# Kernel optimization log

Hardware: AMD Instinct MI355X
Metric: run time of the kernel (lower is better)

## Reference

```python
import jax, jax.numpy as jnp
import numpy as np

DIM = 1024
HEADS = 16
HEAD_DIM = DIM // HEADS
BLOCK = 32
FEAT = 128
EPS = 1e-8


def setup_inputs() -> dict:
    key = jax.random.key(0)
    ks = jax.random.split(key, 5)
    b, n = 4, 4096
    x = jax.random.normal(ks[0], (b, n, DIM), dtype=jnp.float32)
    Wqkv = jax.random.normal(ks[1], (DIM, 3 * DIM), dtype=jnp.float32) / np.sqrt(DIM)
    proj = jax.random.normal(ks[2], (HEADS, HEAD_DIM, FEAT), dtype=jnp.float32) / np.sqrt(HEAD_DIM)
    Wout = jax.random.normal(ks[3], (DIM, DIM), dtype=jnp.float32) / np.sqrt(DIM)
    bout = jnp.zeros((DIM,), dtype=jnp.float32)
    return {"x": x, "Wqkv": Wqkv, "proj": proj, "Wout": Wout, "bout": bout}


def reference(x, Wqkv, proj, Wout, bout):
    b, n, d = x.shape
    h, dh = HEADS, HEAD_DIM
    nb = n // BLOCK
    qkv = x @ Wqkv                                    # [b, n, 3d]
    q, k, v = jnp.split(qkv, 3, axis=-1)
    # [b, h, nb, bs, dh]
    def to_blocks(t):
        return t.reshape(b, nb, BLOCK, h, dh).transpose(0, 3, 1, 2, 4)
    q, k, v = to_blocks(q), to_blocks(k), to_blocks(v)
    # per-head feature projection + elu feature map
    qf = jax.nn.elu(jnp.einsum('bhmsd,hdf->bhmsf', q, proj)) + 1.0
    kf = jax.nn.elu(jnp.einsum('bhmsd,hdf->bhmsf', k, proj)) + 1.0
    kv = jnp.einsum('bhmsf,bhmsd->bhmfd', kf, v)      # per-block kv state
    out = jnp.einsum('bhmsf,bhmfd->bhmsd', qf, kv)
    z = 1.0 / (jnp.einsum('bhmsf,bhmf->bhms', qf, kf.sum(axis=3)) + EPS)
    out = out * z[..., None]
    out = out.transpose(0, 2, 3, 1, 4).reshape(b, n, d)  # [b, n, d]
    return out @ Wout + bout
```

## Files before the change

### kernel.cpp

```cpp
#include <hip/hip_runtime.h>
#include <stdint.h>


typedef unsigned short u16;
typedef __attribute__((ext_vector_type(4))) float f32x4;
typedef __attribute__((ext_vector_type(8))) __bf16 bf16x8;
typedef __attribute__((ext_vector_type(8))) u16 us8;
typedef __attribute__((ext_vector_type(4))) u16 us4;

#define GLOAD_LDS16(g, l)                                                      \
  __builtin_amdgcn_global_load_lds(                                            \
      (const __attribute__((address_space(1))) void*)(g),                      \
      (__attribute__((address_space(3))) void*)(l), 16, 0, 0)

__device__ __forceinline__ u16 f2bf(float f) {
  union { float f; unsigned u; } x; x.f = f;
  return (u16)((x.u + 0x7fffu + ((x.u >> 16) & 1u)) >> 16);
}

__device__ __forceinline__ bf16x8 ld8(const void* p) {
  return __builtin_bit_cast(bf16x8, *(const us8*)p);
}

__device__ __forceinline__ f32x4 mfma16(bf16x8 a, bf16x8 b, f32x4 c) {
  return __builtin_amdgcn_mfma_f32_16x16x32_bf16(a, b, c, 0, 0, 0);
}

__global__ void cast_bf16_k(const float* __restrict__ in, u16* __restrict__ out,
                            int n4) {
  int stride = gridDim.x * blockDim.x;
  for (int i = blockIdx.x * blockDim.x + threadIdx.x; i < n4; i += stride) {
    f32x4 v = ((const f32x4*)in)[i];
    us4 o;
    o[0] = f2bf(v[0]); o[1] = f2bf(v[1]); o[2] = f2bf(v[2]); o[3] = f2bf(v[3]);
    ((us4*)out)[i] = o;
  }
}

__global__ __launch_bounds__(256)
void tcast_k(const float* __restrict__ in, u16* __restrict__ out, int R, int C) {
  __shared__ float tile[32][33];
  int tx = threadIdx.x & 31, ty = threadIdx.x >> 5;
  int r0 = blockIdx.y * 32, c0 = blockIdx.x * 32;
#pragma unroll
  for (int i = 0; i < 32; i += 8)
    tile[ty + i][tx] = in[(size_t)(r0 + ty + i) * C + c0 + tx];
  __syncthreads();
#pragma unroll
  for (int i = 0; i < 32; i += 8)
    out[(size_t)(c0 + ty + i) * R + r0 + tx] = f2bf(tile[tx][ty + i]);
}

__global__ __launch_bounds__(256)
void tcastv_k(const float* __restrict__ Wqkv, u16* __restrict__ dst) {
  __shared__ float tile[32][33];
  int tx = threadIdx.x & 31, ty = threadIdx.x >> 5;
  int e0 = blockIdx.y * 32, j0 = blockIdx.x * 32;
#pragma unroll
  for (int i = 0; i < 32; i += 8)
    tile[ty + i][tx] = Wqkv[(size_t)(e0 + ty + i) * 3072 + 2048 + j0 + tx];
  __syncthreads();
#pragma unroll
  for (int i = 0; i < 32; i += 8)
    dst[(size_t)(j0 + ty + i) * 1024 + e0 + tx] = f2bf(tile[tx][ty + i]);
}

__global__ __launch_bounds__(256)
void wqpb_k(const float* __restrict__ Wqkv, const float* __restrict__ proj,
            u16* __restrict__ BtAll) {
  __shared__ float pl[64][128];
  const int ec = blockIdx.x, h = blockIdx.y, qk = blockIdx.z;
  const float* ph = proj + (size_t)h * 8192;
  for (int i = threadIdx.x; i < 2048; i += 256)
    ((f32x4*)&pl[0][0])[i] = ((const f32x4*)ph)[i];
  __syncthreads();
  const int e = ec * 128 + (threadIdx.x >> 1);
  const int f0 = (threadIdx.x & 1) * 64;
  float wrow[64];
  const float* src = Wqkv + (size_t)e * 3072 + qk * 1024 + h * 64;
#pragma unroll
  for (int i = 0; i < 16; ++i)
    *(f32x4*)&wrow[i * 4] = *(const f32x4*)&src[i * 4];
  u16* dst = BtAll + (size_t)(qk * 2048 + h * 128) * 1024 + e;
  for (int fg = 0; fg < 16; ++fg) {
    f32x4 acc = (f32x4){0.f, 0.f, 0.f, 0.f};
    const int f = f0 + fg * 4;
#pragma unroll
    for (int d = 0; d < 64; ++d) {
      f32x4 p = *(f32x4*)&pl[d][f];
      acc += wrow[d] * p;
    }
#pragma unroll
    for (int u = 0; u < 4; ++u) dst[(size_t)(f + u) * 1024] = f2bf(acc[u]);
  }
}

template <int EPI>
__global__ __launch_bounds__(512, 1)
void gemm8p_k(const u16* __restrict__ A, int lda,
              const u16* __restrict__ Bt, int ldb,
              const float* __restrict__ bias,
              u16* __restrict__ o_qkf, u16* __restrict__ o_v,
              float* __restrict__ o_f32, int K, int ntx) {
  __shared__ __align__(16) char lds[131072];
  const int tid = threadIdx.x, lane = tid & 63, w = tid >> 6;
  const int wm = w >> 2, wn = w & 3;
  const int lr = lane & 15, lg = lane >> 4;
  const int cpx = (int)gridDim.x >> 3;
  const int bid = blockIdx.x;
  const int s = (bid & 7) * cpx + (bid >> 3);
  const int bxN = (s % ntx) * 256;
  const int byM = (s / ntx) * 256;
  const int nt = K >> 6;

  const int srow = w * 8 + (lane >> 3);
  const int scol = ((lane & 7) ^ ((lane >> 3) & 7)) * 8;

  auto stg = [&](const u16* src, int ld, int row0, int kt, int dstoff) {
#pragma unroll
    for (int j = 0; j < 2; ++j)
      GLOAD_LDS16(src + (size_t)(row0 + j * 64 + srow) * ld + kt + scol,
                  lds + dstoff + j * 8192 + w * 1024);
  };
  auto stgA0 = [&](int t) { stg(A, lda, byM, t * 64, (t & 1) * 65536); };
  auto stgA1 = [&](int t) { stg(A, lda, byM + 128, t * 64, (t & 1) * 65536 + 16384); };
  auto stgB0 = [&](int t) { stg(Bt, ldb, bxN, t * 64, (t & 1) * 65536 + 32768); };
  auto stgB1 = [&](int t) { stg(Bt, ldb, bxN + 128, t * 64, (t & 1) * 65536 + 49152); };

  f32x4 acc[8][4];
#pragma unroll
  for (int i = 0; i < 8; ++i)
#pragma unroll
    for (int j = 0; j < 4; ++j) acc[i][j] = (f32x4){0.f, 0.f, 0.f, 0.f};

  stgA0(0); stgA1(0); stgB0(0); stgB1(0);
  if (nt > 1) {
    stgB0(1); stgB1(1);
    asm volatile("s_waitcnt vmcnt(4)" ::: "memory");
  } else {
    asm volatile("s_waitcnt vmcnt(0)" ::: "memory");
  }
  __builtin_amdgcn_s_barrier();

  for (int t = 0; t < nt; ++t) {
    const char* Ab = lds + (t & 1) * 65536 + wm * 16384;
    const char* Bb = lds + (t & 1) * 65536 + 32768 + (wn >> 1) * 16384;
    const int brow = (wn & 1) * 64;
    bf16x8 a2[4][2], b2[4][2];

#pragma unroll
    for (int i = 0; i < 4; ++i)
#pragma unroll
      for (int ks = 0; ks < 2; ++ks) {
        int row = i * 16 + lr;
        a2[i][ks] = ld8(Ab + row * 128 + ((ks * 64 + lg * 16) ^ ((row & 7) << 4)));
      }
#pragma unroll
    for (int j = 0; j < 2; ++j)
#pragma unroll
      for (int ks = 0; ks < 2; ++ks) {
        int row = brow + j * 16 + lr;
        b2[j][ks] = ld8(Bb + row * 128 + ((ks * 64 + lg * 16) ^ ((row & 7) << 4)));
      }
    if (t + 1 < nt) stgA0(t + 1);
    __builtin_amdgcn_s_barrier();
    asm volatile("s_waitcnt lgkmcnt(0)" ::: "memory");
    __builtin_amdgcn_sched_barrier(0);
    __builtin_amdgcn_s_setprio(1);
#pragma unroll
    for (int i = 0; i < 4; ++i)
#pragma unroll
      for (int j = 0; j < 2; ++j)
#pragma unroll
        for (int ks = 0; ks < 2; ++ks)
          acc[i][j] = mfma16(a2[i][ks], b2[j][ks], acc[i][j]);
    __builtin_amdgcn_s_setprio(0);
    __builtin_amdgcn_s_barrier();

#pragma unroll
    for (int j = 2; j < 4; ++j)
#pragma unroll
      for (int ks = 0; ks < 2; ++ks) {
        int row = brow + j * 16 + lr;
        b2[j][ks] = ld8(Bb + row * 128 + ((ks * 64 + lg * 16) ^ ((row & 7) << 4)));
      }
    if (t + 1 < nt) stgA1(t + 1);
    __builtin_amdgcn_s_barrier();
    asm volatile("s_waitcnt lgkmcnt(0)" ::: "memory");
    __builtin_amdgcn_sched_barrier(0);
    __builtin_amdgcn_s_setprio(1);
#pragma unroll
    for (int i = 0; i < 4; ++i)
#pragma unroll
      for (int j = 2; j < 4; ++j)
#pragma unroll
        for (int ks = 0; ks < 2; ++ks)
          acc[i][j] = mfma16(a2[i][ks], b2[j][ks], acc[i][j]);
    __builtin_amdgcn_s_setprio(0);
    __builtin_amdgcn_s_barrier();

#pragma unroll
    for (int i = 0; i < 4; ++i)
#pragma unroll
      for (int ks = 0; ks < 2; ++ks) {
        int row = (4 + i) * 16 + lr;
        a2[i][ks] = ld8(Ab + row * 128 + ((ks * 64 + lg * 16) ^ ((row & 7) << 4)));
      }
    if (t + 2 < nt) stgB0(t + 2);
    __builtin_amdgcn_s_barrier();
    asm volatile("s_waitcnt lgkmcnt(0)" ::: "memory");
    __builtin_amdgcn_sched_barrier(0);
    __builtin_amdgcn_s_setprio(1);
#pragma unroll
    for (int i = 0; i < 4; ++i)
#pragma unroll
      for (int j = 0; j < 2; ++j)
#pragma unroll
        for (int ks = 0; ks < 2; ++ks)
          acc[4 + i][j] = mfma16(a2[i][ks], b2[j][ks], acc[4 + i][j]);
    __builtin_amdgcn_s_setprio(0);
    __builtin_amdgcn_s_barrier();

    if (t + 2 < nt) stgB1(t + 2);
    if (t < nt - 2)
      asm volatile("s_waitcnt vmcnt(4)" ::: "memory");
    else
      asm volatile("s_waitcnt vmcnt(0)" ::: "memory");
    __builtin_amdgcn_s_barrier();
    __builtin_amdgcn_s_setprio(1);
#pragma unroll
    for (int i = 0; i < 4; ++i)
#pragma unroll
      for (int j = 2; j < 4; ++j)
#pragma unroll
        for (int ks = 0; ks < 2; ++ks)
          acc[4 + i][j] = mfma16(a2[i][ks], b2[j][ks], acc[4 + i][j]);
    __builtin_amdgcn_s_setprio(0);
    __builtin_amdgcn_s_barrier();
  }

  const bool doelu = (EPI == 0) && (bxN < 4096);
#pragma unroll
  for (int mi = 0; mi < 8; ++mi)
#pragma unroll
    for (int nj = 0; nj < 4; ++nj) {
      const int col = bxN + wn * 64 + nj * 16 + lr;
#pragma unroll
      for (int rr = 0; rr < 4; ++rr) {
        const int row = byM + wm * 128 + mi * 16 + lg * 4 + rr;
        float x = acc[mi][nj][rr];
        if (EPI == 0) {
          if (doelu) {
            float v = x > 0.f ? x + 1.f : __expf(x);
            o_qkf[(size_t)row * 4096 + col] = f2bf(v);
          } else {
            o_v[(size_t)row * 1024 + (col - 4096)] = f2bf(x);
          }
        } else {
          o_f32[(size_t)row * 1024 + col] = x + bias[col];
        }
      }
    }
}

__global__ __launch_bounds__(64)
void attn_lite_k(const u16* __restrict__ qkf, u16* __restrict__ vbuf) {
  __shared__ __align__(16) u16 V_l[32 * 72];
  __shared__ __align__(16) u16 S_l[32 * 32];
  const int lane = threadIdx.x;
  const int bid = blockIdx.x;
  const int m = bid & 127, h = (bid >> 7) & 15, b = bid >> 11;
  const size_t t0 = (size_t)b * 4096 + (size_t)m * 32;
  const u16* qf = qkf + t0 * 4096 + h * 128;
  const u16* kf = qf + 2048;
  u16* vv = vbuf + t0 * 1024 + h * 64;
  const int lr = lane & 15, lg = lane >> 4;

#pragma unroll
  for (int it = 0; it < 4; ++it) {
    int s2 = it * 8 + (lane >> 3);
    int d0 = (lane & 7) * 8;
    *(us8*)&V_l[s2 * 72 + d0] = *(const us8*)&vv[(size_t)s2 * 1024 + d0];
  }

  f32x4 sacc[2][2];
#pragma unroll
  for (int mm = 0; mm < 2; ++mm)
#pragma unroll
    for (int nn = 0; nn < 2; ++nn) sacc[mm][nn] = (f32x4){0.f, 0.f, 0.f, 0.f};
#pragma unroll
  for (int ks = 0; ks < 4; ++ks) {
    bf16x8 aq[2], bk[2];
#pragma unroll
    for (int mm = 0; mm < 2; ++mm) {
      aq[mm] = ld8(&qf[(size_t)(mm * 16 + lr) * 4096 + ks * 32 + lg * 8]);
      bk[mm] = ld8(&kf[(size_t)(mm * 16 + lr) * 4096 + ks * 32 + lg * 8]);
    }
#pragma unroll
    for (int mm = 0; mm < 2; ++mm)
#pragma unroll
      for (int nn = 0; nn < 2; ++nn)
        sacc[mm][nn] = mfma16(aq[mm], bk[nn], sacc[mm][nn]);
  }

  float rs[2][4];
#pragma unroll
  for (int mm = 0; mm < 2; ++mm)
#pragma unroll
    for (int r = 0; r < 4; ++r) {
      float t = sacc[mm][0][r] + sacc[mm][1][r];
      t += __shfl_xor(t, 1);
      t += __shfl_xor(t, 2);
      t += __shfl_xor(t, 4);
      t += __shfl_xor(t, 8);
      rs[mm][r] = t;
    }

#pragma unroll
  for (int mm = 0; mm < 2; ++mm)
#pragma unroll
    for (int nn = 0; nn < 2; ++nn)
#pragma unroll
      for (int r = 0; r < 4; ++r) {
        int row = mm * 16 + lg * 4 + r;
        int byi = (nn * 16 + lr) * 2;
        *(u16*)((char*)S_l + row * 64 + (byi ^ ((row & 3) << 4))) =
            f2bf(sacc[mm][nn][r]);
      }

  bf16x8 vfr[4];
#pragma unroll
  for (int nn = 0; nn < 4; ++nn) {
    us8 g;
#pragma unroll
    for (int j = 0; j < 8; ++j) g[j] = V_l[(lg * 8 + j) * 72 + nn * 16 + lr];
    vfr[nn] = __builtin_bit_cast(bf16x8, g);
  }
  f32x4 pacc[2][4];
#pragma unroll
  for (int mm = 0; mm < 2; ++mm)
#pragma unroll
    for (int nn = 0; nn < 4; ++nn) pacc[mm][nn] = (f32x4){0.f, 0.f, 0.f, 0.f};
#pragma unroll
  for (int mm = 0; mm < 2; ++mm) {
    int row = mm * 16 + lr;
    int byi = lg * 16;
    bf16x8 a = ld8((char*)S_l + row * 64 + (byi ^ ((row & 3) << 4)));
#pragma unroll
    for (int nn = 0; nn < 4; ++nn) pacc[mm][nn] = mfma16(a, vfr[nn], pacc[mm][nn]);
  }

#pragma unroll
  for (int mm = 0; mm < 2; ++mm)
#pragma unroll
    for (int r = 0; r < 4; ++r) {
      float z = 1.f / (rs[mm][r] + 1e-8f);
      int q = mm * 16 + lg * 4 + r;
#pragma unroll
      for (int nn = 0; nn < 4; ++nn)
        vv[(size_t)q * 1024 + nn * 16 + lr] = f2bf(pacc[mm][nn][r] * z);
    }
}

extern "C" void kernel_launch(void* const* d_in, const int* in_sizes, int n_in,
                              void* d_out, int out_size, void* d_ws,
                              size_t ws_size, hipStream_t stream) {
  const float* x = (const float*)d_in[0];
  const float* Wqkv = (const float*)d_in[1];
  const float* proj = (const float*)d_in[2];
  const float* Wout = (const float*)d_in[3];
  const float* bout = (const float*)d_in[4];
  float* out = (float*)d_out;

  char* ws = (char*)d_ws;
  char* doc = (char*)d_out;

  u16* xb    = (u16*)doc;
  u16* btall = (u16*)(doc + 33554432);
  u16* qkf   = (u16*)ws;
  u16* vbuf  = (u16*)(ws + 134217728);
  u16* woutT = (u16*)(ws + 167772160);

  cast_bf16_k<<<2048, 256, 0, stream>>>(x, xb, 4194304);
  tcastv_k<<<dim3(32, 32), 256, 0, stream>>>(Wqkv, btall + (size_t)4096 * 1024);
  wqpb_k<<<dim3(8, 16, 2), 256, 0, stream>>>(Wqkv, proj, btall);
  tcast_k<<<dim3(32, 32), 256, 0, stream>>>(Wout, woutT, 1024, 1024);

  gemm8p_k<0><<<1280, 512, 0, stream>>>(xb, 1024, btall, 1024, nullptr,
                                        qkf, vbuf, nullptr, 1024, 20);

  attn_lite_k<<<8192, 64, 0, stream>>>(qkf, vbuf);

  gemm8p_k<1><<<256, 512, 0, stream>>>(vbuf, 1024, woutT, 1024, bout,
                                       nullptr, nullptr, out, 1024, 4);
}
```

Before: 427.3 us.

## Restructure GEMM main loop into two phases with fewer barriers

Collapses the four-phase, ping-pong style GEMM inner loop into two phases. Each phase loads the full B fragment set once and half of A, then issues all 32 MFMAs for that half. Global-to-LDS prefetches for A(t+1) and B(t+2) are now issued in pairs. This drops six of the eight barriers per iteration along with the explicit lgkmcnt waits, sched_barrier and setprio hints, cutting sync overhead. The cost is losing the fine-grained interleaving of LDS reads with MFMA work and holding more fragment registers live, which could lower occupancy.

Measured after the change: 418.3 us. 2.1% less time.

```diff
diff --git a/kernel.cpp b/kernel.cpp
--- a/kernel.cpp
+++ b/kernel.cpp
@@ -146,96 +146,51 @@
     const char* Ab = lds + (t & 1) * 65536 + wm * 16384;
     const char* Bb = lds + (t & 1) * 65536 + 32768 + (wn >> 1) * 16384;
     const int brow = (wn & 1) * 64;
-    bf16x8 a2[4][2], b2[4][2];
-
+    bf16x8 alo[4][2], ahi[4][2], bl[4][2];
+
+    if (t + 1 < nt) { stgA0(t + 1); stgA1(t + 1); }
 #pragma unroll
     for (int i = 0; i < 4; ++i)
 #pragma unroll
       for (int ks = 0; ks < 2; ++ks) {
         int row = i * 16 + lr;
-        a2[i][ks] = ld8(Ab + row * 128 + ((ks * 64 + lg * 16) ^ ((row & 7) << 4)));
-      }
-#pragma unroll
-    for (int j = 0; j < 2; ++j)
+        alo[i][ks] = ld8(Ab + row * 128 + ((ks * 64 + lg * 16) ^ ((row & 7) << 4)));
+      }
+#pragma unroll
+    for (int j = 0; j < 4; ++j)
 #pragma unroll
       for (int ks = 0; ks < 2; ++ks) {
         int row = brow + j * 16 + lr;
-        b2[j][ks] = ld8(Bb + row * 128 + ((ks * 64 + lg * 16) ^ ((row & 7) << 4)));
-      }
-    if (t + 1 < nt) stgA0(t + 1);
+        bl[j][ks] = ld8(Bb + row * 128 + ((ks * 64 + lg * 16) ^ ((row & 7) << 4)));
+      }
+#pragma unroll
+    for (int i = 0; i < 4; ++i)
+#pragma unroll
+      for (int j = 0; j < 4; ++j)
+#pragma unroll
+        for (int ks = 0; ks < 2; ++ks)
+          acc[i][j] = mfma16(alo[i][ks], bl[j][ks], acc[i][j]);
     __builtin_amdgcn_s_barrier();
-    asm volatile("s_waitcnt lgkmcnt(0)" ::: "memory");
-    __builtin_amdgcn_sched_barrier(0);
-    __builtin_amdgcn_s_setprio(1);
-#pragma unroll
-    for (int i = 0; i < 4; ++i)
-#pragma unroll
-      for (int j = 0; j < 2; ++j)
-#pragma unroll
-        for (int ks = 0; ks < 2; ++ks)
-          acc[i][j] = mfma16(a2[i][ks], b2[j][ks], acc[i][j]);
-    __builtin_amdgcn_s_setprio(0);
-    __builtin_amdgcn_s_barrier();
-
-#pragma unroll
-    for (int j = 2; j < 4; ++j)
-#pragma unroll
-      for (int ks = 0; ks < 2; ++ks) {
-        int row = brow + j * 16 + lr;
-        b2[j][ks] = ld8(Bb + row * 128 + ((ks * 64 + lg * 16) ^ ((row & 7) << 4)));
-      }
-    if (t + 1 < nt) stgA1(t + 1);
-    __builtin_amdgcn_s_barrier();
-    asm volatile("s_waitcnt lgkmcnt(0)" ::: "memory");
-    __builtin_amdgcn_sched_barrier(0);
-    __builtin_amdgcn_s_setprio(1);
-#pragma unroll
-    for (int i = 0; i < 4; ++i)
-#pragma unroll
-      for (int j = 2; j < 4; ++j)
-#pragma unroll
-        for (int ks = 0; ks < 2; ++ks)
-          acc[i][j] = mfma16(a2[i][ks], b2[j][ks], acc[i][j]);
-    __builtin_amdgcn_s_setprio(0);
-    __builtin_amdgcn_s_barrier();
-
+
+    if (t + 2 < nt) { stgB0(t + 2); stgB1(t + 2); }
 #pragma unroll
     for (int i = 0; i < 4; ++i)
 #pragma unroll
       for (int ks = 0; ks < 2; ++ks) {
         int row = (4 + i) * 16 + lr;
-        a2[i][ks] = ld8(Ab + row * 128 + ((ks * 64 + lg * 16) ^ ((row & 7) << 4)));
-      }
-    if (t + 2 < nt) stgB0(t + 2);
-    __builtin_amdgcn_s_barrier();
-    asm volatile("s_waitcnt lgkmcnt(0)" ::: "memory");
-    __builtin_amdgcn_sched_barrier(0);
-    __builtin_amdgcn_s_setprio(1);
+        ahi[i][ks] = ld8(Ab + row * 128 + ((ks * 64 + lg * 16) ^ ((row & 7) << 4)));
+      }
 #pragma unroll
     for (int i = 0; i < 4; ++i)
 #pragma unroll
-      for (int j = 0; j < 2; ++j)
+      for (int j = 0; j < 4; ++j)
 #pragma unroll
         for (int ks = 0; ks < 2; ++ks)
-          acc[4 + i][j] = mfma16(a2[i][ks], b2[j][ks], acc[4 + i][j]);
-    __builtin_amdgcn_s_setprio(0);
-    __builtin_amdgcn_s_barrier();
-
-    if (t + 2 < nt) stgB1(t + 2);
+          acc[4 + i][j] = mfma16(ahi[i][ks], bl[j][ks], acc[4 + i][j]);
     if (t < nt - 2)
       asm volatile("s_waitcnt vmcnt(4)" ::: "memory");
     else
       asm volatile("s_waitcnt vmcnt(0)" ::: "memory");
-    __builtin_amdgcn_s_barrier();
-    __builtin_amdgcn_s_setprio(1);
-#pragma unroll
-    for (int i = 0; i < 4; ++i)
-#pragma unroll
-      for (int j = 2; j < 4; ++j)
-#pragma unroll
-        for (int ks = 0; ks < 2; ++ks)
-          acc[4 + i][j] = mfma16(a2[i][ks], b2[j][ks], acc[4 + i][j]);
-    __builtin_amdgcn_s_setprio(0);
     __builtin_amdgcn_s_barrier();
   }
 
```
